# Performance work log

Hardware: AMD Instinct MI355X
Metric: run time of the kernel (lower is better)

Reference implementation:

```python
import jax, jax.numpy as jnp
import numpy as np

N = 100000      # particles
E = 1600000     # particle pairs
B = 1024        # jets (batch); max(part_indicator)+1
C_IN = 64
HID = 32
T = 4           # n_terms
MID = 128
OUT = 128
EPS = 1e-5


def setup_inputs() -> dict:
    key = jax.random.key(0)
    ks = jax.random.split(key, 10)
    s = 0.05
    return {
        "part_features": jax.random.normal(ks[0], (N, C_IN), jnp.float32),
        "part_weight": jax.random.uniform(ks[1], (N, 1), jnp.float32),
        "pair_func": jax.random.normal(ks[2], (E, T), jnp.float32),
        "pair_head": jax.random.randint(ks[3], (E, 1), 0, N),
        "pair_tail": jax.random.randint(ks[4], (E, 1), 0, N),
        "part_indicator": jax.random.randint(ks[5], (N, 1), 0, B),
        "W_sc": jax.random.normal(ks[6], (OUT, C_IN), jnp.float32) * s,
        "g1": jnp.ones((C_IN,), jnp.float32), "b1": jnp.zeros((C_IN,), jnp.float32),
        "W1": jax.random.normal(ks[7], (HID, C_IN), jnp.float32) * s,
        "g2": jnp.ones((T * HID,), jnp.float32), "b2": jnp.zeros((T * HID,), jnp.float32),
        "W2": jax.random.normal(ks[8], (MID, T * HID), jnp.float32) * s,
        "g3": jnp.ones((MID,), jnp.float32), "b3": jnp.zeros((MID,), jnp.float32),
        "W3": jax.random.normal(ks[9], (OUT, MID), jnp.float32) * s,
    }


def weighted_bn(x, w, ind, gamma, beta):
    # segment-sum weighted features per jet -> batch stats over jets (training mode)
    jet = jax.ops.segment_sum(x * w, ind, num_segments=B)  # [B, C]
    mean = jet.mean(0)
    var = jet.var(0, ddof=1)  # unbiased, matches torch var(0, unbiased=True)
    return (x - mean) / jnp.sqrt(var + EPS) * gamma + beta


def reference(part_features, part_weight, pair_func, pair_head, pair_tail,
              part_indicator, W_sc, g1, b1, W1, g2, b2, W2, g3, b3, W3):
    ind = part_indicator[:, 0]
    head = pair_head[:, 0]
    tail = pair_tail[:, 0]

    short_cut = part_features @ W_sc.T                       # [N, OUT]

    h = jax.nn.relu(weighted_bn(part_features, part_weight, ind, g1, b1))
    h = h @ W1.T                                             # [N, HID]
    h = h * part_weight

    # gather tail features, expand by polynomial terms, scatter-add to head
    msg = (h[tail][:, :, None] * pair_func[:, None, :T]).reshape(E, HID * T)
    agg = jax.ops.segment_sum(msg, head, num_segments=N)     # [N, HID*T]

    h = jax.nn.relu(weighted_bn(agg, part_weight, ind, g2, b2)) @ W2.T  # [N, MID]
    h = jax.nn.relu(weighted_bn(h, part_weight, ind, g3, b3)) @ W3.T    # [N, OUT]
    return h + short_cut
```

## Files before the change

### kernel.cpp

```cpp
#include <hip/hip_runtime.h>

#define N_NODES 100000
#define N_EDGES 1600000
#define NB      1024
#define EPSF    1e-5f

#define SCHUNK 128
#define SNBLK ((N_NODES + SCHUNK - 1) / SCHUNK)

#define BUK_SH  7
#define NBUK    ((N_NODES + 127) >> 7)
#define EPB     16384
#define NBA     ((N_EDGES + EPB - 1) / EPB)
#define NCB     (NBUK * NBA)
#define SNB2    ((NCB + SCHUNK - 1) / SCHUNK)

typedef float f32x4  __attribute__((ext_vector_type(4)));
typedef short bf16x8 __attribute__((ext_vector_type(8)));

__device__ __forceinline__ float bf2f(unsigned short u) {
    union { unsigned int i; float f; } v; v.i = ((unsigned int)u) << 16; return v.f;
}
__device__ __forceinline__ unsigned short f2bf(float f) {
    union { float ff; unsigned int i; } v; v.ff = f;
    unsigned int r = v.i + 0x7FFFu + ((v.i >> 16) & 1u);
    return (unsigned short)(r >> 16);
}

template<int C>
__global__ __launch_bounds__(256) void stats_kernel(const float* __restrict__ jet,
                                                    const float* __restrict__ g,
                                                    const float* __restrict__ b,
                                                    float* __restrict__ scale,
                                                    float* __restrict__ shift) {
    int c = blockIdx.x;
    int t = threadIdx.x;
    float s = 0.f, s2 = 0.f;
    for (int r = t; r < NB; r += 256) {
        float v = jet[r * C + c];
        s += v; s2 += v * v;
    }
    __shared__ float ls[256], ls2[256];
    ls[t] = s; ls2[t] = s2;
    __syncthreads();
    for (int ofs = 128; ofs > 0; ofs >>= 1) {
        if (t < ofs) { ls[t] += ls[t + ofs]; ls2[t] += ls2[t + ofs]; }
        __syncthreads();
    }
    if (t == 0) {
        float mean = ls[0] / (float)NB;
        float var  = (ls2[0] - (float)NB * mean * mean) / (float)(NB - 1);
        float sc   = g[c] / sqrtf(var + EPSF);
        scale[c] = sc;
        shift[c] = b[c] - mean * sc;
    }
}

__global__ __launch_bounds__(256) void countI_kernel(const int* __restrict__ ind,
                                                     int* __restrict__ cntI) {
    int n = blockIdx.x * 256 + threadIdx.x;
    if (n < N_NODES) atomicAdd(&cntI[ind[n]], 1);
}

__global__ __launch_bounds__(256) void count_head_kernel(const int* __restrict__ head,
                                                         int* __restrict__ cnt) {
    int e = blockIdx.x * 256 + threadIdx.x;
    if (e < N_EDGES) atomicAdd(&cnt[head[e]], 1);
}

__global__ __launch_bounds__(1024) void countCB_kernel(const int* __restrict__ head,
                                                       int* __restrict__ cnt_cb) {
    __shared__ int h[NBUK];
    int tid = threadIdx.x;
    int blk = blockIdx.x;
    for (int i = tid; i < NBUK; i += 1024) h[i] = 0;
    __syncthreads();
    int e0 = blk * EPB;
    for (int k = tid; k < EPB; k += 1024) {
        int e = e0 + k;
        if (e < N_EDGES) atomicAdd(&h[head[e] >> BUK_SH], 1);
    }
    __syncthreads();
    for (int i = tid; i < NBUK; i += 1024) cnt_cb[i * NBA + blk] = h[i];
}

__global__ __launch_bounds__(SCHUNK) void scanA_kernel(const int* __restrict__ cnt,
                                                       int* __restrict__ part, int n) {
    __shared__ int ls[SCHUNK];
    int t = threadIdx.x;
    int i = blockIdx.x * SCHUNK + t;
    ls[t] = (i < n) ? cnt[i] : 0;
    __syncthreads();
    for (int ofs = SCHUNK / 2; ofs > 0; ofs >>= 1) {
        if (t < ofs) ls[t] += ls[t + ofs];
        __syncthreads();
    }
    if (t == 0) part[blockIdx.x] = ls[0];
}

__global__ __launch_bounds__(1024) void scanB_kernel(const int* __restrict__ in,
                                                     int* __restrict__ out,
                                                     int* __restrict__ out2, int n) {
    __shared__ int ls[1024];
    int t = threadIdx.x;
    int v = (t < n) ? in[t] : 0;
    ls[t] = v;
    __syncthreads();
    for (int ofs = 1; ofs < 1024; ofs <<= 1) {
        int u = (t >= ofs) ? ls[t - ofs] : 0;
        __syncthreads();
        ls[t] += u;
        __syncthreads();
    }
    if (t < n) {
        int e = ls[t] - v;
        out[t] = e;
        if (out2) out2[t] = e;
    }
}

__global__ __launch_bounds__(SCHUNK) void scanC_kernel(const int* __restrict__ cnt,
                                                       const int* __restrict__ poff,
                                                       int* __restrict__ base,
                                                       int* __restrict__ cursor, int n) {
    __shared__ int ls[SCHUNK];
    int t = threadIdx.x;
    int i = blockIdx.x * SCHUNK + t;
    int v = (i < n) ? cnt[i] : 0;
    ls[t] = v;
    __syncthreads();
    for (int ofs = 1; ofs < SCHUNK; ofs <<= 1) {
        int u = (t >= ofs) ? ls[t - ofs] : 0;
        __syncthreads();
        ls[t] += u;
        __syncthreads();
    }
    if (i < n) {
        int bse = poff[blockIdx.x] + ls[t] - v;
        base[i] = bse;
        cursor[i] = bse;
    }
}

__global__ __launch_bounds__(1024) void binC16_kernel(const int* __restrict__ head,
                                                      const int* __restrict__ tail,
                                                      const float* __restrict__ pf,
                                                      const int* __restrict__ cbase,
                                                      uint4* __restrict__ hb16) {
    __shared__ int cur[NBUK];
    int tid = threadIdx.x;
    int blk = blockIdx.x;
    for (int i = tid; i < NBUK; i += 1024) cur[i] = cbase[i * NBA + blk];
    __syncthreads();
    int e0 = blk * EPB;
    for (int k = tid; k < EPB; k += 1024) {
        int e = e0 + k;
        if (e < N_EDGES) {
            int hd = head[e];
            int b = hd >> BUK_SH;
            int slot = atomicAdd(&cur[b], 1);
            float4 pv = ((const float4*)pf)[e];
            uint4 rec;
            rec.x = (unsigned)tail[e] | ((unsigned)(hd & 127) << 21);
            rec.y = (unsigned)f2bf(pv.x) | ((unsigned)f2bf(pv.y) << 16);
            rec.z = (unsigned)f2bf(pv.z) | ((unsigned)f2bf(pv.w) << 16);
            rec.w = 0u;
            hb16[slot] = rec;
        }
    }
}

__global__ __launch_bounds__(512) void sortD2_kernel(const int* __restrict__ cbase,
                                                     const uint4* __restrict__ hb16,
                                                     int* __restrict__ base_e,
                                                     int* __restrict__ cnt_e,
                                                     int* __restrict__ tail_s,
                                                     uint2* __restrict__ pf_s8) {
    __shared__ int hcnt[128];
    __shared__ int hscan[128];
    int tid = threadIdx.x;
    int b = blockIdx.x;
    int lo = cbase[b * NBA];
    int hi = (b + 1 < NBUK) ? cbase[(b + 1) * NBA] : N_EDGES;
    if (tid < 128) hcnt[tid] = 0;
    __syncthreads();
    for (int k = lo + tid; k < hi; k += 512) {
        unsigned rx = ((const unsigned*)hb16)[(size_t)k * 4];
        atomicAdd(&hcnt[rx >> 21], 1);
    }
    __syncthreads();
    if (tid < 128) hscan[tid] = hcnt[tid];
    __syncthreads();
    for (int ofs = 1; ofs < 128; ofs <<= 1) {
        int v = (tid < 128 && tid >= ofs) ? hscan[tid - ofs] : 0;
        __syncthreads();
        if (tid < 128) hscan[tid] += v;
        __syncthreads();
    }
    if (tid < 128) {
        int h = (b << BUK_SH) + tid;
        int bse = lo + hscan[tid] - hcnt[tid];
        if (h < N_NODES) { base_e[h] = bse; cnt_e[h] = hcnt[tid]; }
        hscan[tid] = bse;
    }
    __syncthreads();
    for (int k = lo + tid; k < hi; k += 512) {
        uint4 rec = hb16[k];
        int h7 = (int)(rec.x >> 21);
        int slot = atomicAdd(&hscan[h7], 1);
        tail_s[slot] = (int)(rec.x & 0xFFFFFu);
        pf_s8[slot] = make_uint2(rec.y, rec.z);
    }
}

__global__ __launch_bounds__(256) void escatterE_kernel(const int* __restrict__ head,
                                                        int* __restrict__ cursor,
                                                        int* __restrict__ eid) {
    int e = blockIdx.x * 256 + threadIdx.x;
    if (e >= N_EDGES) return;
    int slot = atomicAdd(&cursor[head[e]], 1);
    eid[slot] = e;
}

__global__ __launch_bounds__(256) void scatterI_kernel(const int* __restrict__ ind,
                                                       int* __restrict__ cursorI,
                                                       int* __restrict__ order) {
    int n = blockIdx.x * 256 + threadIdx.x;
    if (n < N_NODES) {
        int pos = atomicAdd(&cursorI[ind[n]], 1);
        order[pos] = n;
    }
}

template<int C>
__global__ __launch_bounds__(256) void bucket_jet_kernel(const float* __restrict__ xx,
                                                         const float* __restrict__ w,
                                                         const int* __restrict__ order,
                                                         const int* __restrict__ baseI,
                                                         const int* __restrict__ cntI,
                                                         float* __restrict__ jet) {
    constexpr int G = 256 / C;
    __shared__ float red[256];
    int b = blockIdx.x;
    int g = threadIdx.x / C;
    int c = threadIdx.x % C;
    int s0 = baseI[b], m = cntI[b];
    float s = 0.f;
    for (int k = g; k < m; k += G) {
        int n = order[s0 + k];
        s += xx[(size_t)n * C + c] * w[n];
    }
    red[threadIdx.x] = s;
    __syncthreads();
    for (int half = G / 2; half > 0; half >>= 1) {
        if (g < half) red[g * C + c] += red[(g + half) * C + c];
        __syncthreads();
    }
    if (g == 0) jet[b * C + c] = red[c];
}

__global__ __launch_bounds__(256) void bucket_jet_bf128_kernel(const unsigned short* __restrict__ xx,
                                                               const float* __restrict__ w,
                                                               const int* __restrict__ order,
                                                               const int* __restrict__ baseI,
                                                               const int* __restrict__ cntI,
                                                               float* __restrict__ jet) {
    __shared__ float redA[256], redB[256];
    int b = blockIdx.x;
    int g  = threadIdx.x >> 6;
    int c2 = threadIdx.x & 63;
    int s0 = baseI[b], m = cntI[b];
    float a0 = 0.f, a1 = 0.f;
    for (int k = g; k < m; k += 4) {
        int n = order[s0 + k];
        float wn = w[n];
        unsigned u = ((const unsigned*)xx)[(size_t)n * 64 + c2];
        a0 += bf2f((unsigned short)(u & 0xFFFFu)) * wn;
        a1 += bf2f((unsigned short)(u >> 16)) * wn;
    }
    redA[threadIdx.x] = a0; redB[threadIdx.x] = a1;
    __syncthreads();
    for (int half = 2; half > 0; half >>= 1) {
        if (g < half) {
            redA[g * 64 + c2] += redA[(g + half) * 64 + c2];
            redB[g * 64 + c2] += redB[(g + half) * 64 + c2];
        }
        __syncthreads();
    }
    if (g == 0) {
        jet[b * 128 + 2 * c2]     = redA[c2];
        jet[b * 128 + 2 * c2 + 1] = redB[c2];
    }
}

#define TILE1 64
__global__ __launch_bounds__(256) void fused1_kernel(const float* __restrict__ x,
                                                     const float* __restrict__ w,
                                                     const float* __restrict__ scale,
                                                     const float* __restrict__ shift,
                                                     const float* __restrict__ W1,
                                                     unsigned short* __restrict__ hs) {
    __shared__ __align__(16) unsigned short xnb[TILE1 * 64];
    __shared__ __align__(16) unsigned short w1b[32 * 64];
    int tid = threadIdx.x;
    int n0  = blockIdx.x * TILE1;
    char* xnb_ = (char*)xnb; char* w1b_ = (char*)w1b;

    for (int idx = tid; idx < TILE1 * 8; idx += 256) {
        int r = idx >> 3, c0 = (idx & 7) << 3;
        int n = n0 + r;
        float4 vA = make_float4(0.f, 0.f, 0.f, 0.f), vB = vA;
        if (n < N_NODES) {
            vA = *(const float4*)&x[(size_t)n * 64 + c0];
            vB = *(const float4*)&x[(size_t)n * 64 + c0 + 4];
        }
        float4 scA = *(const float4*)&scale[c0], scB = *(const float4*)&scale[c0 + 4];
        float4 shA = *(const float4*)&shift[c0], shB = *(const float4*)&shift[c0 + 4];
        unsigned short na[8];
        na[0] = f2bf(fmaxf(fmaf(vA.x, scA.x, shA.x), 0.f));
        na[1] = f2bf(fmaxf(fmaf(vA.y, scA.y, shA.y), 0.f));
        na[2] = f2bf(fmaxf(fmaf(vA.z, scA.z, shA.z), 0.f));
        na[3] = f2bf(fmaxf(fmaf(vA.w, scA.w, shA.w), 0.f));
        na[4] = f2bf(fmaxf(fmaf(vB.x, scB.x, shB.x), 0.f));
        na[5] = f2bf(fmaxf(fmaf(vB.y, scB.y, shB.y), 0.f));
        na[6] = f2bf(fmaxf(fmaf(vB.z, scB.z, shB.z), 0.f));
        na[7] = f2bf(fmaxf(fmaf(vB.w, scB.w, shB.w), 0.f));
        int byte = ((r << 7) + ((idx & 7) << 4)) ^ ((r & 7) << 4);
        *(bf16x8*)(xnb_ + byte) = *(bf16x8*)na;
    }
    for (int idx = tid; idx < 32 * 8; idx += 256) {
        int r = idx >> 3, c0 = (idx & 7) << 3;
        float4 vA = *(const float4*)&W1[(size_t)r * 64 + c0];
        float4 vB = *(const float4*)&W1[(size_t)r * 64 + c0 + 4];
        unsigned short ua[8];
        ua[0] = f2bf(vA.x); ua[1] = f2bf(vA.y); ua[2] = f2bf(vA.z); ua[3] = f2bf(vA.w);
        ua[4] = f2bf(vB.x); ua[5] = f2bf(vB.y); ua[6] = f2bf(vB.z); ua[7] = f2bf(vB.w);
        int byte = ((r << 7) + ((idx & 7) << 4)) ^ ((r & 7) << 4);
        *(bf16x8*)(w1b_ + byte) = *(bf16x8*)ua;
    }
    __syncthreads();

    int wv   = tid >> 6;
    int lane = tid & 63;
    int l15  = lane & 15;
    int lhi  = lane >> 4;

    f32x4 acc[2];
    acc[0] = (f32x4){0.f, 0.f, 0.f, 0.f};
    acc[1] = (f32x4){0.f, 0.f, 0.f, 0.f};

#pragma unroll
    for (int ks = 0; ks < 2; ks++) {
        int rA = (wv << 4) + l15;
        int byteA = ((rA << 7) + (ks << 6) + (lhi << 4)) ^ ((rA & 7) << 4);
        bf16x8 a = *(const bf16x8*)(xnb_ + byteA);
#pragma unroll
        for (int cf = 0; cf < 2; cf++) {
            int rB = (cf << 4) + l15;
            int byteB = ((rB << 7) + (ks << 6) + (lhi << 4)) ^ ((rB & 7) << 4);
            bf16x8 b = *(const bf16x8*)(w1b_ + byteB);
            acc[cf] = __builtin_amdgcn_mfma_f32_16x16x32_bf16(a, b, acc[cf], 0, 0, 0);
        }
    }

#pragma unroll
    for (int cf = 0; cf < 2; cf++) {
        int co = (cf << 4) + l15;
#pragma unroll
        for (int j = 0; j < 4; j++) {
            int n = n0 + (wv << 4) + (lhi << 2) + j;
            if (n < N_NODES) hs[(size_t)n * 32 + co] = f2bf(acc[cf][j] * w[n]);
        }
    }
}

template<int PRE>
__global__ __launch_bounds__(256) void gather2_kernel(const int* __restrict__ base,
                                                      const int* __restrict__ cnt,
                                                      const int* __restrict__ tail_s,
                                                      const unsigned* __restrict__ pf_s8,
                                                      const int* __restrict__ eid,
                                                      const int* __restrict__ tail,
                                                      const float* __restrict__ pf,
                                                      const unsigned short* __restrict__ hs,
                                                      unsigned short* __restrict__ agg) {
    int n = blockIdx.x * 4 + (threadIdx.x >> 6);
    if (n >= N_NODES) return;
    int lane = threadIdx.x & 63;
    int i = lane >> 1;
    int half = lane & 1;
    int s0 = base[n], c = cnt[n];
    float a0 = 0.f, a1 = 0.f;
    int k = 0;
    for (; k + 4 <= c; k += 4) {
        int t0, t1, t2, t3;
        float2 p0, p1, p2, p3;
        if (PRE) {
            t0 = tail_s[s0 + k];     t1 = tail_s[s0 + k + 1];
            t2 = tail_s[s0 + k + 2]; t3 = tail_s[s0 + k + 3];
            unsigned u0 = pf_s8[(size_t)(s0 + k) * 2 + half];
            unsigned u1 = pf_s8[(size_t)(s0 + k + 1) * 2 + half];
            unsigned u2 = pf_s8[(size_t)(s0 + k + 2) * 2 + half];
            unsigned u3 = pf_s8[(size_t)(s0 + k + 3) * 2 + half];
            p0 = make_float2(bf2f((unsigned short)(u0 & 0xFFFFu)), bf2f((unsigned short)(u0 >> 16)));
            p1 = make_float2(bf2f((unsigned short)(u1 & 0xFFFFu)), bf2f((unsigned short)(u1 >> 16)));
            p2 = make_float2(bf2f((unsigned short)(u2 & 0xFFFFu)), bf2f((unsigned short)(u2 >> 16)));
            p3 = make_float2(bf2f((unsigned short)(u3 & 0xFFFFu)), bf2f((unsigned short)(u3 >> 16)));
        } else {
            int e0 = eid[s0 + k],     e1 = eid[s0 + k + 1];
            int e2 = eid[s0 + k + 2], e3 = eid[s0 + k + 3];
            t0 = tail[e0]; t1 = tail[e1]; t2 = tail[e2]; t3 = tail[e3];
            p0 = *(const float2*)&pf[(size_t)e0 * 4 + half * 2];
            p1 = *(const float2*)&pf[(size_t)e1 * 4 + half * 2];
            p2 = *(const float2*)&pf[(size_t)e2 * 4 + half * 2];
            p3 = *(const float2*)&pf[(size_t)e3 * 4 + half * 2];
        }
        float h0 = bf2f(hs[(size_t)t0 * 32 + i]);
        float h1 = bf2f(hs[(size_t)t1 * 32 + i]);
        float h2 = bf2f(hs[(size_t)t2 * 32 + i]);
        float h3 = bf2f(hs[(size_t)t3 * 32 + i]);
        a0 += h0 * p0.x; a1 += h0 * p0.y;
        a0 += h1 * p1.x; a1 += h1 * p1.y;
        a0 += h2 * p2.x; a1 += h2 * p2.y;
        a0 += h3 * p3.x; a1 += h3 * p3.y;
    }
    for (; k < c; k++) {
        int t0; float2 p0;
        if (PRE) {
            t0 = tail_s[s0 + k];
            unsigned u0 = pf_s8[(size_t)(s0 + k) * 2 + half];
            p0 = make_float2(bf2f((unsigned short)(u0 & 0xFFFFu)), bf2f((unsigned short)(u0 >> 16)));
        } else {
            int e0 = eid[s0 + k];
            t0 = tail[e0];
            p0 = *(const float2*)&pf[(size_t)e0 * 4 + half * 2];
        }
        float h0 = bf2f(hs[(size_t)t0 * 32 + i]);
        a0 += h0 * p0.x; a1 += h0 * p0.y;
    }
    unsigned pk = (unsigned)f2bf(a0) | ((unsigned)f2bf(a1) << 16);
    ((unsigned*)agg)[(size_t)n * 64 + lane] = pk;
}

__global__ __launch_bounds__(256) void edge_kernel(const int* __restrict__ head,
                                                   const int* __restrict__ tail,
                                                   const float* __restrict__ pf,
                                                   const unsigned short* __restrict__ hs,
                                                   float* __restrict__ agg) {
    long long tid = (long long)blockIdx.x * 256 + threadIdx.x;
    if (tid >= (long long)N_EDGES * 128) return;
    int e = (int)(tid >> 7);
    int j = (int)(tid & 127);
    int i = j >> 2, t = j & 3;
    float v = bf2f(hs[(size_t)tail[e] * 32 + i]) * pf[(size_t)e * 4 + t];
    atomicAdd(&agg[(size_t)head[e] * 128 + j], v);
}

#define TILE2 64
template<int INBF, int OUTBF>
__global__ __launch_bounds__(256) void fused2_kernel(const void* __restrict__ xin_,
                                                     const float* __restrict__ scale,
                                                     const float* __restrict__ shift,
                                                     const float* __restrict__ W,
                                                     void* __restrict__ yout_) {
    __shared__ __align__(16) unsigned short xnb[TILE2 * 128];
    __shared__ __align__(16) unsigned short wb[128 * 128];
    int tid = threadIdx.x;
    int n0  = blockIdx.x * TILE2;
    char* xbase = (char*)xnb;
    char* wbase = (char*)wb;

    for (int idx = tid; idx < TILE2 * 16; idx += 256) {
        int r = idx >> 4;
        int c0 = (idx & 15) << 3;
        int n = n0 + r;
        float f[8];
        if (n < N_NODES) {
            if (INBF) {
                const unsigned short* xu = (const unsigned short*)xin_;
                uint4 U = *(const uint4*)(xu + (size_t)n * 128 + c0);
                f[0] = bf2f((unsigned short)(U.x & 0xFFFFu)); f[1] = bf2f((unsigned short)(U.x >> 16));
                f[2] = bf2f((unsigned short)(U.y & 0xFFFFu)); f[3] = bf2f((unsigned short)(U.y >> 16));
                f[4] = bf2f((unsigned short)(U.z & 0xFFFFu)); f[5] = bf2f((unsigned short)(U.z >> 16));
                f[6] = bf2f((unsigned short)(U.w & 0xFFFFu)); f[7] = bf2f((unsigned short)(U.w >> 16));
            } else {
                const float* xf = (const float*)xin_;
                float4 vA = *(const float4*)&xf[(size_t)n * 128 + c0];
                float4 vB = *(const float4*)&xf[(size_t)n * 128 + c0 + 4];
                f[0] = vA.x; f[1] = vA.y; f[2] = vA.z; f[3] = vA.w;
                f[4] = vB.x; f[5] = vB.y; f[6] = vB.z; f[7] = vB.w;
            }
        } else {
#pragma unroll
            for (int q = 0; q < 8; q++) f[q] = 0.f;
        }
        unsigned short ua[8];
#pragma unroll
        for (int q = 0; q < 8; q++)
            ua[q] = f2bf(fmaxf(fmaf(f[q], scale[c0 + q], shift[c0 + q]), 0.f));
        int byte = ((r << 8) + ((idx & 15) << 4)) ^ ((r & 7) << 4);
        *(bf16x8*)(xbase + byte) = *(bf16x8*)ua;
    }
    for (int idx = tid; idx < 128 * 16; idx += 256) {
        int r = idx >> 4;
        int c0 = (idx & 15) << 3;
        float4 vA = *(const float4*)&W[(size_t)r * 128 + c0];
        float4 vB = *(const float4*)&W[(size_t)r * 128 + c0 + 4];
        unsigned short ua[8];
        ua[0] = f2bf(vA.x); ua[1] = f2bf(vA.y); ua[2] = f2bf(vA.z); ua[3] = f2bf(vA.w);
        ua[4] = f2bf(vB.x); ua[5] = f2bf(vB.y); ua[6] = f2bf(vB.z); ua[7] = f2bf(vB.w);
        int byte = ((r << 8) + ((idx & 15) << 4)) ^ ((r & 7) << 4);
        *(bf16x8*)(wbase + byte) = *(bf16x8*)ua;
    }
    __syncthreads();

    int wv   = tid >> 6;
    int lane = tid & 63;
    int l15  = lane & 15;
    int lhi  = lane >> 4;

    f32x4 acc[8];
#pragma unroll
    for (int cf = 0; cf < 8; cf++) acc[cf] = (f32x4){0.f, 0.f, 0.f, 0.f};

#pragma unroll
    for (int ks = 0; ks < 4; ks++) {
        int rA = (wv << 4) + l15;
        int byteA = ((rA << 8) + (ks << 6) + (lhi << 4)) ^ ((rA & 7) << 4);
        bf16x8 a = *(const bf16x8*)(xbase + byteA);
#pragma unroll
        for (int cf = 0; cf < 8; cf++) {
            int rB = (cf << 4) + l15;
            int byteB = ((rB << 8) + (ks << 6) + (lhi << 4)) ^ ((rB & 7) << 4);
            bf16x8 b = *(const bf16x8*)(wbase + byteB);
            acc[cf] = __builtin_amdgcn_mfma_f32_16x16x32_bf16(a, b, acc[cf], 0, 0, 0);
        }
    }

#pragma unroll
    for (int cf = 0; cf < 8; cf++) {
        int col = (cf << 4) + l15;
#pragma unroll
        for (int j = 0; j < 4; j++) {
            int n = n0 + (wv << 4) + (lhi << 2) + j;
            if (n < N_NODES) {
                float v = acc[cf][j];
                if (OUTBF) ((unsigned short*)yout_)[(size_t)n * 128 + col] = f2bf(v);
                else       ((float*)yout_)[(size_t)n * 128 + col] = v;
            }
        }
    }
}

template<int INBF>
__global__ __launch_bounds__(256) void fused3_kernel(const void* __restrict__ h2_,
                                                     const float* __restrict__ x,
                                                     const float* __restrict__ scale,
                                                     const float* __restrict__ shift,
                                                     const float* __restrict__ Wsc,
                                                     const float* __restrict__ W3,
                                                     float* __restrict__ out) {
    __shared__ __align__(16) unsigned short xnb[TILE2 * 128];
    __shared__ __align__(16) unsigned short xrb[TILE2 * 64];
    __shared__ __align__(16) unsigned short wb[128 * 128];
    int tid = threadIdx.x;
    int n0  = blockIdx.x * TILE2;
    char* xbase = (char*)xnb;
    char* rbase = (char*)xrb;
    char* wbase = (char*)wb;

    for (int idx = tid; idx < TILE2 * 16; idx += 256) {
        int r = idx >> 4;
        int c0 = (idx & 15) << 3;
        int n = n0 + r;
        float f[8];
        if (n < N_NODES) {
            if (INBF) {
                const unsigned short* xu = (const unsigned short*)h2_;
                uint4 U = *(const uint4*)(xu + (size_t)n * 128 + c0);
                f[0] = bf2f((unsigned short)(U.x & 0xFFFFu)); f[1] = bf2f((unsigned short)(U.x >> 16));
                f[2] = bf2f((unsigned short)(U.y & 0xFFFFu)); f[3] = bf2f((unsigned short)(U.y >> 16));
                f[4] = bf2f((unsigned short)(U.z & 0xFFFFu)); f[5] = bf2f((unsigned short)(U.z >> 16));
                f[6] = bf2f((unsigned short)(U.w & 0xFFFFu)); f[7] = bf2f((unsigned short)(U.w >> 16));
            } else {
                const float* xf = (const float*)h2_;
                float4 vA = *(const float4*)&xf[(size_t)n * 128 + c0];
                float4 vB = *(const float4*)&xf[(size_t)n * 128 + c0 + 4];
                f[0] = vA.x; f[1] = vA.y; f[2] = vA.z; f[3] = vA.w;
                f[4] = vB.x; f[5] = vB.y; f[6] = vB.z; f[7] = vB.w;
            }
        } else {
#pragma unroll
            for (int q = 0; q < 8; q++) f[q] = 0.f;
        }
        unsigned short ua[8];
#pragma unroll
        for (int q = 0; q < 8; q++)
            ua[q] = f2bf(fmaxf(fmaf(f[q], scale[c0 + q], shift[c0 + q]), 0.f));
        int byte = ((r << 8) + ((idx & 15) << 4)) ^ ((r & 7) << 4);
        *(bf16x8*)(xbase + byte) = *(bf16x8*)ua;
    }
    for (int idx = tid; idx < TILE2 * 8; idx += 256) {
        int r = idx >> 3, c0 = (idx & 7) << 3;
        int n = n0 + r;
        float4 vA = make_float4(0.f, 0.f, 0.f, 0.f), vB = vA;
        if (n < N_NODES) {
            vA = *(const float4*)&x[(size_t)n * 64 + c0];
            vB = *(const float4*)&x[(size_t)n * 64 + c0 + 4];
        }
        unsigned short ua[8];
        ua[0] = f2bf(vA.x); ua[1] = f2bf(vA.y); ua[2] = f2bf(vA.z); ua[3] = f2bf(vA.w);
        ua[4] = f2bf(vB.x); ua[5] = f2bf(vB.y); ua[6] = f2bf(vB.z); ua[7] = f2bf(vB.w);
        int byte = ((r << 7) + ((idx & 7) << 4)) ^ ((r & 7) << 4);
        *(bf16x8*)(rbase + byte) = *(bf16x8*)ua;
    }
    for (int idx = tid; idx < 128 * 8; idx += 256) {
        int r = idx >> 3, c0 = (idx & 7) << 3;
        float4 vA = *(const float4*)&Wsc[(size_t)r * 64 + c0];
        float4 vB = *(const float4*)&Wsc[(size_t)r * 64 + c0 + 4];
        unsigned short ua[8];
        ua[0] = f2bf(vA.x); ua[1] = f2bf(vA.y); ua[2] = f2bf(vA.z); ua[3] = f2bf(vA.w);
        ua[4] = f2bf(vB.x); ua[5] = f2bf(vB.y); ua[6] = f2bf(vB.z); ua[7] = f2bf(vB.w);
        int byte = ((r << 7) + ((idx & 7) << 4)) ^ ((r & 7) << 4);
        *(bf16x8*)(wbase + byte) = *(bf16x8*)ua;
    }
    __syncthreads();

    int wv   = tid >> 6;
    int lane = tid & 63;
    int l15  = lane & 15;
    int lhi  = lane >> 4;

    f32x4 acc[8];
#pragma unroll
    for (int cf = 0; cf < 8; cf++) acc[cf] = (f32x4){0.f, 0.f, 0.f, 0.f};

#pragma unroll
    for (int ks = 0; ks < 2; ks++) {
        int rA = (wv << 4) + l15;
        int byteA = ((rA << 7) + (ks << 6) + (lhi << 4)) ^ ((rA & 7) << 4);
        bf16x8 a = *(const bf16x8*)(rbase + byteA);
#pragma unroll
        for (int cf = 0; cf < 8; cf++) {
            int rB = (cf << 4) + l15;
            int byteB = ((rB << 7) + (ks << 6) + (lhi << 4)) ^ ((rB & 7) << 4);
            bf16x8 b = *(const bf16x8*)(wbase + byteB);
            acc[cf] = __builtin_amdgcn_mfma_f32_16x16x32_bf16(a, b, acc[cf], 0, 0, 0);
        }
    }
    __syncthreads();
    for (int idx = tid; idx < 128 * 16; idx += 256) {
        int r = idx >> 4;
        int c0 = (idx & 15) << 3;
        float4 vA = *(const float4*)&W3[(size_t)r * 128 + c0];
        float4 vB = *(const float4*)&W3[(size_t)r * 128 + c0 + 4];
        unsigned short ua[8];
        ua[0] = f2bf(vA.x); ua[1] = f2bf(vA.y); ua[2] = f2bf(vA.z); ua[3] = f2bf(vA.w);
        ua[4] = f2bf(vB.x); ua[5] = f2bf(vB.y); ua[6] = f2bf(vB.z); ua[7] = f2bf(vB.w);
        int byte = ((r << 8) + ((idx & 15) << 4)) ^ ((r & 7) << 4);
        *(bf16x8*)(wbase + byte) = *(bf16x8*)ua;
    }
    __syncthreads();

#pragma unroll
    for (int ks = 0; ks < 4; ks++) {
        int rA = (wv << 4) + l15;
        int byteA = ((rA << 8) + (ks << 6) + (lhi << 4)) ^ ((rA & 7) << 4);
        bf16x8 a = *(const bf16x8*)(xbase + byteA);
#pragma unroll
        for (int cf = 0; cf < 8; cf++) {
            int rB = (cf << 4) + l15;
            int byteB = ((rB << 8) + (ks << 6) + (lhi << 4)) ^ ((rB & 7) << 4);
            bf16x8 b = *(const bf16x8*)(wbase + byteB);
            acc[cf] = __builtin_amdgcn_mfma_f32_16x16x32_bf16(a, b, acc[cf], 0, 0, 0);
        }
    }

#pragma unroll
    for (int cf = 0; cf < 8; cf++) {
        int col = (cf << 4) + l15;
#pragma unroll
        for (int j = 0; j < 4; j++) {
            int n = n0 + (wv << 4) + (lhi << 2) + j;
            if (n < N_NODES) out[(size_t)n * 128 + col] = acc[cf][j];
        }
    }
}

extern "C" void kernel_launch(void* const* d_in, const int* in_sizes, int n_in,
                              void* d_out, int out_size, void* d_ws, size_t ws_size,
                              hipStream_t stream) {
    const float* x    = (const float*)d_in[0];
    const float* w    = (const float*)d_in[1];
    const float* pf   = (const float*)d_in[2];
    const int*   head = (const int*)d_in[3];
    const int*   tail = (const int*)d_in[4];
    const int*   ind  = (const int*)d_in[5];
    const float* Wsc  = (const float*)d_in[6];
    const float* g1   = (const float*)d_in[7];
    const float* b1   = (const float*)d_in[8];
    const float* W1   = (const float*)d_in[9];
    const float* g2   = (const float*)d_in[10];
    const float* b2   = (const float*)d_in[11];
    const float* W2   = (const float*)d_in[12];
    const float* g3   = (const float*)d_in[13];
    const float* b3   = (const float*)d_in[14];
    const float* W3   = (const float*)d_in[15];
    float* out = (float*)d_out;

    char* p = (char*)d_ws;
    unsigned short* hs = (unsigned short*)p;  p += (size_t)N_NODES * 32 * 2;
    char* aggraw = p;                         p += (size_t)N_NODES * 128 * 4;
    unsigned short* agg_bf = (unsigned short*)aggraw;
    float*          agg_f  = (float*)aggraw;
    uint4* hb16 = (uint4*)(aggraw + (size_t)N_NODES * 128 * 2);
    float* jet1 = (float*)p;                  p += 1024 * 64 * 4;
    float* jet2 = (float*)p;                  p += 1024 * 128 * 4;
    float* jet3 = (float*)p;                  p += 1024 * 128 * 4;
    float* sc1 = (float*)p; p += 64 * 4;  float* sh1 = (float*)p; p += 64 * 4;
    float* sc2 = (float*)p; p += 128 * 4; float* sh2 = (float*)p; p += 128 * 4;
    float* sc3 = (float*)p; p += 128 * 4; float* sh3 = (float*)p; p += 128 * 4;
    int* cnt_e    = (int*)p; p += (size_t)N_NODES * 4;
    int* base_e   = (int*)p; p += (size_t)N_NODES * 4;
    int* cursor_e = (int*)p; p += (size_t)N_NODES * 4;
    int* part     = (int*)p; p += 1024 * 4;
    int* cntI     = (int*)p; p += 1024 * 4;
    int* baseI    = (int*)p; p += 1024 * 4;
    int* cursorI  = (int*)p; p += 1024 * 4;
    int* order    = (int*)p; p += (size_t)N_NODES * 4;
    int* eid      = (int*)p; p += (size_t)N_EDGES * 4;
    size_t need_t2 = (size_t)(p - (char*)d_ws);
    int* cnt_cb   = (int*)p; p += (size_t)NCB * 4;
    int* cbase    = (int*)p; p += (size_t)NCB * 4;
    int* ccur     = (int*)p; p += (size_t)NCB * 4;
    int*   tail_s = (int*)p;   p += (size_t)N_EDGES * 4;
    uint2* pf_s8  = (uint2*)p; p += (size_t)N_EDGES * 8;
    size_t need_t1 = (size_t)(p - (char*)d_ws);
    int tier = (ws_size >= need_t1) ? 1 : (ws_size >= need_t2) ? 2 : 3;

    hipMemsetAsync(cntI, 0, 1024 * sizeof(int), stream);
    countI_kernel<<<(N_NODES + 255) / 256, 256, 0, stream>>>(ind, cntI);
    scanB_kernel<<<1, 1024, 0, stream>>>(cntI, baseI, cursorI, 1024);
    scatterI_kernel<<<(N_NODES + 255) / 256, 256, 0, stream>>>(ind, cursorI, order);

    bucket_jet_kernel<64><<<1024, 256, 0, stream>>>(x, w, order, baseI, cntI, jet1);
    stats_kernel<64><<<64, 256, 0, stream>>>(jet1, g1, b1, sc1, sh1);

    fused1_kernel<<<(N_NODES + TILE1 - 1) / TILE1, 256, 0, stream>>>(
        x, w, sc1, sh1, W1, hs);

    if (tier == 1) {
        countCB_kernel<<<NBA, 1024, 0, stream>>>(head, cnt_cb);
        scanA_kernel<<<SNB2, SCHUNK, 0, stream>>>(cnt_cb, part, NCB);
        scanB_kernel<<<1, 1024, 0, stream>>>(part, part, nullptr, SNB2);
        scanC_kernel<<<SNB2, SCHUNK, 0, stream>>>(cnt_cb, part, cbase, ccur, NCB);
        binC16_kernel<<<NBA, 1024, 0, stream>>>(head, tail, pf, cbase, hb16);
        sortD2_kernel<<<NBUK, 512, 0, stream>>>(cbase, hb16, base_e, cnt_e,
                                                tail_s, pf_s8);
        gather2_kernel<1><<<(N_NODES + 3) / 4, 256, 0, stream>>>(
            base_e, cnt_e, tail_s, (const unsigned*)pf_s8, nullptr, tail, pf, hs, agg_bf);
    } else if (tier == 2) {
        hipMemsetAsync(cnt_e, 0, N_NODES * sizeof(int), stream);
        count_head_kernel<<<(N_EDGES + 255) / 256, 256, 0, stream>>>(head, cnt_e);
        scanA_kernel<<<SNBLK, SCHUNK, 0, stream>>>(cnt_e, part, N_NODES);
        scanB_kernel<<<1, 1024, 0, stream>>>(part, part, nullptr, SNBLK);
        scanC_kernel<<<SNBLK, SCHUNK, 0, stream>>>(cnt_e, part, base_e, cursor_e, N_NODES);
        escatterE_kernel<<<(N_EDGES + 255) / 256, 256, 0, stream>>>(
            head, cursor_e, eid);
        gather2_kernel<0><<<(N_NODES + 3) / 4, 256, 0, stream>>>(
            base_e, cnt_e, nullptr, nullptr, eid, tail, pf, hs, agg_bf);
    }

    if (tier <= 2) {
        bucket_jet_bf128_kernel<<<1024, 256, 0, stream>>>(agg_bf, w, order, baseI, cntI, jet2);
        stats_kernel<128><<<128, 256, 0, stream>>>(jet2, g2, b2, sc2, sh2);
        fused2_kernel<1, 1><<<(N_NODES + TILE2 - 1) / TILE2, 256, 0, stream>>>(
            agg_bf, sc2, sh2, W2, agg_bf);
        bucket_jet_bf128_kernel<<<1024, 256, 0, stream>>>(agg_bf, w, order, baseI, cntI, jet3);
        stats_kernel<128><<<128, 256, 0, stream>>>(jet3, g3, b3, sc3, sh3);
        fused3_kernel<1><<<(N_NODES + TILE2 - 1) / TILE2, 256, 0, stream>>>(
            agg_bf, x, sc3, sh3, Wsc, W3, out);
    } else {
        hipMemsetAsync(agg_f, 0, (size_t)N_NODES * 128 * sizeof(float), stream);
        edge_kernel<<<(int)(((long long)N_EDGES * 128) / 256), 256, 0, stream>>>(
            head, tail, pf, hs, agg_f);
        bucket_jet_kernel<128><<<1024, 256, 0, stream>>>(agg_f, w, order, baseI, cntI, jet2);
        stats_kernel<128><<<128, 256, 0, stream>>>(jet2, g2, b2, sc2, sh2);
        fused2_kernel<0, 0><<<(N_NODES + TILE2 - 1) / TILE2, 256, 0, stream>>>(
            agg_f, sc2, sh2, W2, agg_f);
        bucket_jet_kernel<128><<<1024, 256, 0, stream>>>(agg_f, w, order, baseI, cntI, jet3);
        stats_kernel<128><<<128, 256, 0, stream>>>(jet3, g3, b3, sc3, sh3);
        fused3_kernel<0><<<(N_NODES + TILE2 - 1) / TILE2, 256, 0, stream>>>(
            agg_f, x, sc3, sh3, Wsc, W3, out);
    }

    (void)in_sizes; (void)n_in; (void)out_size;
}
```

Measured before the change: 318.1 us.

## Fuse per-bucket sort with gather aggregation using shared-memory staging

The bucket sort pass and the gather pass are merged into one kernel: each 128-node bucket counting-sorts its edges into LDS (tail and packed bf16 pair terms), then each wave aggregates 16 heads directly from LDS and writes agg. The binning kernel now writes SoA tail/pf arrays instead of 16-byte records. This drops the global tail_s/pf_s8 round trip and one kernel launch. The trade-offs are 48KB of LDS per block, which limits occupancy, only 8 waves per bucket doing the gather, and a slow quadratic fallback when a bucket exceeds 4096 edges.

```diff
diff --git a/kernel.cpp b/kernel.cpp
--- a/kernel.cpp
+++ b/kernel.cpp
@@ -14,6 +14,7 @@
 #define NBA     ((N_EDGES + EPB - 1) / EPB)
 #define NCB     (NBUK * NBA)
 #define SNB2    ((NCB + SCHUNK - 1) / SCHUNK)
+#define CAP     4096
 
 typedef float f32x4  __attribute__((ext_vector_type(4)));
 typedef short bf16x8 __attribute__((ext_vector_type(8)));
@@ -142,11 +143,12 @@
     }
 }
 
-__global__ __launch_bounds__(1024) void binC16_kernel(const int* __restrict__ head,
+__global__ __launch_bounds__(1024) void binSoA_kernel(const int* __restrict__ head,
                                                       const int* __restrict__ tail,
                                                       const float* __restrict__ pf,
                                                       const int* __restrict__ cbase,
-                                                      uint4* __restrict__ hb16) {
+                                                      unsigned* __restrict__ bt,
+                                                      uint2* __restrict__ bp) {
     __shared__ int cur[NBUK];
     int tid = threadIdx.x;
     int blk = blockIdx.x;
@@ -160,56 +162,118 @@
             int b = hd >> BUK_SH;
             int slot = atomicAdd(&cur[b], 1);
             float4 pv = ((const float4*)pf)[e];
-            uint4 rec;
-            rec.x = (unsigned)tail[e] | ((unsigned)(hd & 127) << 21);
-            rec.y = (unsigned)f2bf(pv.x) | ((unsigned)f2bf(pv.y) << 16);
-            rec.z = (unsigned)f2bf(pv.z) | ((unsigned)f2bf(pv.w) << 16);
-            rec.w = 0u;
-            hb16[slot] = rec;
-        }
-    }
-}
-
-__global__ __launch_bounds__(512) void sortD2_kernel(const int* __restrict__ cbase,
-                                                     const uint4* __restrict__ hb16,
-                                                     int* __restrict__ base_e,
-                                                     int* __restrict__ cnt_e,
-                                                     int* __restrict__ tail_s,
-                                                     uint2* __restrict__ pf_s8) {
+            bt[slot] = (unsigned)tail[e] | ((unsigned)(hd & 127) << 21);
+            bp[slot] = make_uint2(
+                (unsigned)f2bf(pv.x) | ((unsigned)f2bf(pv.y) << 16),
+                (unsigned)f2bf(pv.z) | ((unsigned)f2bf(pv.w) << 16));
+        }
+    }
+}
+
+__global__ __launch_bounds__(512) void sortGather_kernel(const int* __restrict__ cbase,
+                                                         const unsigned* __restrict__ bt,
+                                                         const uint2* __restrict__ bp,
+                                                         const unsigned short* __restrict__ hs,
+                                                         unsigned short* __restrict__ agg) {
     __shared__ int hcnt[128];
-    __shared__ int hscan[128];
+    __shared__ int hbase[128];
+    __shared__ int hcur[128];
+    __shared__ int tail_l[CAP];
+    __shared__ unsigned pf_l[2 * CAP];
     int tid = threadIdx.x;
     int b = blockIdx.x;
     int lo = cbase[b * NBA];
     int hi = (b + 1 < NBUK) ? cbase[(b + 1) * NBA] : N_EDGES;
+    int cnt = hi - lo;
     if (tid < 128) hcnt[tid] = 0;
     __syncthreads();
-    for (int k = lo + tid; k < hi; k += 512) {
-        unsigned rx = ((const unsigned*)hb16)[(size_t)k * 4];
-        atomicAdd(&hcnt[rx >> 21], 1);
-    }
-    __syncthreads();
-    if (tid < 128) hscan[tid] = hcnt[tid];
+    for (int k = lo + tid; k < hi; k += 512)
+        atomicAdd(&hcnt[bt[k] >> 21], 1);
+    __syncthreads();
+    if (tid < 128) hbase[tid] = hcnt[tid];
     __syncthreads();
     for (int ofs = 1; ofs < 128; ofs <<= 1) {
-        int v = (tid < 128 && tid >= ofs) ? hscan[tid - ofs] : 0;
-        __syncthreads();
-        if (tid < 128) hscan[tid] += v;
+        int v = (tid < 128 && tid >= ofs) ? hbase[tid - ofs] : 0;
+        __syncthreads();
+        if (tid < 128) hbase[tid] += v;
         __syncthreads();
     }
     if (tid < 128) {
-        int h = (b << BUK_SH) + tid;
-        int bse = lo + hscan[tid] - hcnt[tid];
-        if (h < N_NODES) { base_e[h] = bse; cnt_e[h] = hcnt[tid]; }
-        hscan[tid] = bse;
-    }
-    __syncthreads();
-    for (int k = lo + tid; k < hi; k += 512) {
-        uint4 rec = hb16[k];
-        int h7 = (int)(rec.x >> 21);
-        int slot = atomicAdd(&hscan[h7], 1);
-        tail_s[slot] = (int)(rec.x & 0xFFFFFu);
-        pf_s8[slot] = make_uint2(rec.y, rec.z);
+        int bse = hbase[tid] - hcnt[tid];
+        hbase[tid] = bse;
+        hcur[tid] = bse;
+    }
+    __syncthreads();
+
+    int wv = tid >> 6, lane = tid & 63;
+    int i = lane >> 1, half = lane & 1;
+
+    if (cnt <= CAP) {
+        for (int k = lo + tid; k < hi; k += 512) {
+            unsigned rx = bt[k];
+            uint2 pv = bp[k];
+            int slot = atomicAdd(&hcur[rx >> 21], 1);
+            tail_l[slot] = (int)(rx & 0xFFFFFu);
+            pf_l[2 * slot]     = pv.x;
+            pf_l[2 * slot + 1] = pv.y;
+        }
+        __syncthreads();
+        for (int j = 0; j < 16; j++) {
+            int h7 = (wv << 4) + j;
+            int n = (b << BUK_SH) + h7;
+            if (n >= N_NODES) break;
+            int s0 = hbase[h7], c = hcnt[h7];
+            float a0 = 0.f, a1 = 0.f;
+            int k = 0;
+            for (; k + 4 <= c; k += 4) {
+                int t0 = tail_l[s0 + k],     t1 = tail_l[s0 + k + 1];
+                int t2 = tail_l[s0 + k + 2], t3 = tail_l[s0 + k + 3];
+                unsigned u0 = pf_l[2 * (s0 + k) + half];
+                unsigned u1 = pf_l[2 * (s0 + k + 1) + half];
+                unsigned u2 = pf_l[2 * (s0 + k + 2) + half];
+                unsigned u3 = pf_l[2 * (s0 + k + 3) + half];
+                float h0 = bf2f(hs[(size_t)t0 * 32 + i]);
+                float h1 = bf2f(hs[(size_t)t1 * 32 + i]);
+                float h2 = bf2f(hs[(size_t)t2 * 32 + i]);
+                float h3 = bf2f(hs[(size_t)t3 * 32 + i]);
+                a0 += h0 * bf2f((unsigned short)(u0 & 0xFFFFu));
+                a1 += h0 * bf2f((unsigned short)(u0 >> 16));
+                a0 += h1 * bf2f((unsigned short)(u1 & 0xFFFFu));
+                a1 += h1 * bf2f((unsigned short)(u1 >> 16));
+                a0 += h2 * bf2f((unsigned short)(u2 & 0xFFFFu));
+                a1 += h2 * bf2f((unsigned short)(u2 >> 16));
+                a0 += h3 * bf2f((unsigned short)(u3 & 0xFFFFu));
+                a1 += h3 * bf2f((unsigned short)(u3 >> 16));
+            }
+            for (; k < c; k++) {
+                int t0 = tail_l[s0 + k];
+                unsigned u0 = pf_l[2 * (s0 + k) + half];
+                float h0 = bf2f(hs[(size_t)t0 * 32 + i]);
+                a0 += h0 * bf2f((unsigned short)(u0 & 0xFFFFu));
+                a1 += h0 * bf2f((unsigned short)(u0 >> 16));
+            }
+            unsigned pk = (unsigned)f2bf(a0) | ((unsigned)f2bf(a1) << 16);
+            ((unsigned*)agg)[(size_t)n * 64 + lane] = pk;
+        }
+    } else {
+        for (int j = 0; j < 16; j++) {
+            int h7 = (wv << 4) + j;
+            int n = (b << BUK_SH) + h7;
+            if (n >= N_NODES) break;
+            unsigned my = (unsigned)h7;
+            float a0 = 0.f, a1 = 0.f;
+            for (int k = lo; k < hi; k++) {
+                unsigned rx = bt[k];
+                if ((rx >> 21) == my) {
+                    unsigned u0 = (half == 0) ? bp[k].x : bp[k].y;
+                    float h0 = bf2f(hs[(size_t)(rx & 0xFFFFFu) * 32 + i]);
+                    a0 += h0 * bf2f((unsigned short)(u0 & 0xFFFFu));
+                    a1 += h0 * bf2f((unsigned short)(u0 >> 16));
+                }
+            }
+            unsigned pk = (unsigned)f2bf(a0) | ((unsigned)f2bf(a1) << 16);
+            ((unsigned*)agg)[(size_t)n * 64 + lane] = pk;
+        }
     }
 }
 
@@ -374,11 +438,8 @@
     }
 }
 
-template<int PRE>
 __global__ __launch_bounds__(256) void gather2_kernel(const int* __restrict__ base,
                                                       const int* __restrict__ cnt,
-                                                      const int* __restrict__ tail_s,
-                                                      const unsigned* __restrict__ pf_s8,
                                                       const int* __restrict__ eid,
                                                       const int* __restrict__ tail,
                                                       const float* __restrict__ pf,
@@ -391,50 +452,10 @@
     int half = lane & 1;
     int s0 = base[n], c = cnt[n];
     float a0 = 0.f, a1 = 0.f;
-    int k = 0;
-    for (; k + 4 <= c; k += 4) {
-        int t0, t1, t2, t3;
-        float2 p0, p1, p2, p3;
-        if (PRE) {
-            t0 = tail_s[s0 + k];     t1 = tail_s[s0 + k + 1];
-            t2 = tail_s[s0 + k + 2]; t3 = tail_s[s0 + k + 3];
-            unsigned u0 = pf_s8[(size_t)(s0 + k) * 2 + half];
-            unsigned u1 = pf_s8[(size_t)(s0 + k + 1) * 2 + half];
-            unsigned u2 = pf_s8[(size_t)(s0 + k + 2) * 2 + half];
-            unsigned u3 = pf_s8[(size_t)(s0 + k + 3) * 2 + half];
-            p0 = make_float2(bf2f((unsigned short)(u0 & 0xFFFFu)), bf2f((unsigned short)(u0 >> 16)));
-            p1 = make_float2(bf2f((unsigned short)(u1 & 0xFFFFu)), bf2f((unsigned short)(u1 >> 16)));
-            p2 = make_float2(bf2f((unsigned short)(u2 & 0xFFFFu)), bf2f((unsigned short)(u2 >> 16)));
-            p3 = make_float2(bf2f((unsigned short)(u3 & 0xFFFFu)), bf2f((unsigned short)(u3 >> 16)));
-        } else {
-            int e0 = eid[s0 + k],     e1 = eid[s0 + k + 1];
-            int e2 = eid[s0 + k + 2], e3 = eid[s0 + k + 3];
-            t0 = tail[e0]; t1 = tail[e1]; t2 = tail[e2]; t3 = tail[e3];
-            p0 = *(const float2*)&pf[(size_t)e0 * 4 + half * 2];
-            p1 = *(const float2*)&pf[(size_t)e1 * 4 + half * 2];
-            p2 = *(const float2*)&pf[(size_t)e2 * 4 + half * 2];
-            p3 = *(const float2*)&pf[(size_t)e3 * 4 + half * 2];
-        }
-        float h0 = bf2f(hs[(size_t)t0 * 32 + i]);
-        float h1 = bf2f(hs[(size_t)t1 * 32 + i]);
-        float h2 = bf2f(hs[(size_t)t2 * 32 + i]);
-        float h3 = bf2f(hs[(size_t)t3 * 32 + i]);
-        a0 += h0 * p0.x; a1 += h0 * p0.y;
-        a0 += h1 * p1.x; a1 += h1 * p1.y;
-        a0 += h2 * p2.x; a1 += h2 * p2.y;
-        a0 += h3 * p3.x; a1 += h3 * p3.y;
-    }
-    for (; k < c; k++) {
-        int t0; float2 p0;
-        if (PRE) {
-            t0 = tail_s[s0 + k];
-            unsigned u0 = pf_s8[(size_t)(s0 + k) * 2 + half];
-            p0 = make_float2(bf2f((unsigned short)(u0 & 0xFFFFu)), bf2f((unsigned short)(u0 >> 16)));
-        } else {
-            int e0 = eid[s0 + k];
-            t0 = tail[e0];
-            p0 = *(const float2*)&pf[(size_t)e0 * 4 + half * 2];
-        }
+    for (int k = 0; k < c; k++) {
+        int e0 = eid[s0 + k];
+        int t0 = tail[e0];
+        float2 p0 = *(const float2*)&pf[(size_t)e0 * 4 + half * 2];
         float h0 = bf2f(hs[(size_t)t0 * 32 + i]);
         a0 += h0 * p0.x; a1 += h0 * p0.y;
     }
@@ -713,7 +734,8 @@
     char* aggraw = p;                         p += (size_t)N_NODES * 128 * 4;
     unsigned short* agg_bf = (unsigned short*)aggraw;
     float*          agg_f  = (float*)aggraw;
-    uint4* hb16 = (uint4*)(aggraw + (size_t)N_NODES * 128 * 2);
+    unsigned* bt = (unsigned*)(aggraw + (size_t)N_NODES * 128 * 2);
+    uint2*    bp = (uint2*)((char*)bt + (size_t)N_EDGES * 4);
     float* jet1 = (float*)p;                  p += 1024 * 64 * 4;
     float* jet2 = (float*)p;                  p += 1024 * 128 * 4;
     float* jet3 = (float*)p;                  p += 1024 * 128 * 4;
@@ -733,8 +755,6 @@
     int* cnt_cb   = (int*)p; p += (size_t)NCB * 4;
     int* cbase    = (int*)p; p += (size_t)NCB * 4;
     int* ccur     = (int*)p; p += (size_t)NCB * 4;
-    int*   tail_s = (int*)p;   p += (size_t)N_EDGES * 4;
-    uint2* pf_s8  = (uint2*)p; p += (size_t)N_EDGES * 8;
     size_t need_t1 = (size_t)(p - (char*)d_ws);
     int tier = (ws_size >= need_t1) ? 1 : (ws_size >= need_t2) ? 2 : 3;
 
@@ -754,11 +774,8 @@
         scanA_kernel<<<SNB2, SCHUNK, 0, stream>>>(cnt_cb, part, NCB);
         scanB_kernel<<<1, 1024, 0, stream>>>(part, part, nullptr, SNB2);
         scanC_kernel<<<SNB2, SCHUNK, 0, stream>>>(cnt_cb, part, cbase, ccur, NCB);
-        binC16_kernel<<<NBA, 1024, 0, stream>>>(head, tail, pf, cbase, hb16);
-        sortD2_kernel<<<NBUK, 512, 0, stream>>>(cbase, hb16, base_e, cnt_e,
-                                                tail_s, pf_s8);
-        gather2_kernel<1><<<(N_NODES + 3) / 4, 256, 0, stream>>>(
-            base_e, cnt_e, tail_s, (const unsigned*)pf_s8, nullptr, tail, pf, hs, agg_bf);
+        binSoA_kernel<<<NBA, 1024, 0, stream>>>(head, tail, pf, cbase, bt, bp);
+        sortGather_kernel<<<NBUK, 512, 0, stream>>>(cbase, bt, bp, hs, agg_bf);
     } else if (tier == 2) {
         hipMemsetAsync(cnt_e, 0, N_NODES * sizeof(int), stream);
         count_head_kernel<<<(N_EDGES + 255) / 256, 256, 0, stream>>>(head, cnt_e);
@@ -767,8 +784,8 @@
         scanC_kernel<<<SNBLK, SCHUNK, 0, stream>>>(cnt_e, part, base_e, cursor_e, N_NODES);
         escatterE_kernel<<<(N_EDGES + 255) / 256, 256, 0, stream>>>(
             head, cursor_e, eid);
-        gather2_kernel<0><<<(N_NODES + 3) / 4, 256, 0, stream>>>(
-            base_e, cnt_e, nullptr, nullptr, eid, tail, pf, hs, agg_bf);
+        gather2_kernel<<<(N_NODES + 3) / 4, 256, 0, stream>>>(
+            base_e, cnt_e, eid, tail, pf, hs, agg_bf);
     }
 
     if (tier <= 2) {
```

Result: no change. 317.6 us (-0.2%).
